# Performance work log

Measured on AMD Instinct MI355X. Metric: run time of the kernel, lower is better.

Reference implementation:

```python
import jax, jax.numpy as jnp
import numpy as np

B, S, E, H = 2, 2048, 768, 12
HD = E // H
EPS = 1e-5


def setup_inputs() -> dict:
    key = jax.random.key(0)
    ks = jax.random.split(key, 7)
    sc_in = 1.0 / np.sqrt(E)
    return {
        "x": jax.random.normal(ks[0], (B, S, E), dtype=jnp.float32),
        "gamma": jnp.ones((E,), dtype=jnp.float32),
        "beta": jnp.zeros((E,), dtype=jnp.float32),
        "Wqkv": jax.random.normal(ks[1], (3 * E, E), dtype=jnp.float32) * sc_in,
        "bqkv": jax.random.normal(ks[2], (3 * E,), dtype=jnp.float32) * 0.01,
        "Wo": jax.random.normal(ks[3], (E, E), dtype=jnp.float32) * sc_in,
        "bo": jax.random.normal(ks[4], (E,), dtype=jnp.float32) * 0.01,
    }


def reference(x, gamma, beta, Wqkv, bqkv, Wo, bo):
    # LayerNorm
    mu = jnp.mean(x, axis=-1, keepdims=True)
    var = jnp.mean(jnp.square(x - mu), axis=-1, keepdims=True)
    xn = (x - mu) * jax.lax.rsqrt(var + EPS) * gamma + beta
    # fused QKV projection; original reshapes to [B,S,H,3*hd] then chunks,
    # i.e. per-head blocks of 3*hd split into q/k/v slices of hd each.
    qkv = (xn @ Wqkv.T + bqkv).reshape(B, S, H, 3, HD)
    q, k, v = qkv[..., 0, :], qkv[..., 1, :], qkv[..., 2, :]  # [B,S,H,hd]
    scores = jnp.einsum("bshd,bthd->bhst", q, k) / np.sqrt(HD)
    attn = jax.nn.softmax(scores, axis=-1)  # [B,H,S,S]
    out = jnp.einsum("bhst,bthd->bshd", attn, v).reshape(B, S, E)
    return out @ Wo.T + bo
```

## Files before the change

kernel.cpp:

```cpp
#include <hip/hip_runtime.h>
#include <math.h>

#define B_  2
#define S_  2048
#define E_  768
#define H_  12
#define HD_ 64
#define M_  (B_ * S_)
#define N3E (3 * E_)

typedef __attribute__((ext_vector_type(8)))  short short8;
typedef __attribute__((ext_vector_type(8)))  _Float16 half8;
typedef __attribute__((ext_vector_type(4)))  _Float16 half4;
typedef __attribute__((ext_vector_type(2)))  _Float16 half2_t;
typedef __attribute__((ext_vector_type(4)))  float floatx4;
typedef __attribute__((ext_vector_type(16))) float floatx16;

#define QSCALE 0.18033688011112042f

__device__ inline unsigned short f2bf(float f) {
  union { float f; unsigned u; } a; a.f = f;
  unsigned r = a.u + 0x7fff + ((a.u >> 16) & 1);
  return (unsigned short)(r >> 16);
}
__device__ inline unsigned short f2bf_fast(float f) {
  union { float f; unsigned u; } a; a.f = f;
  return (unsigned short)((a.u + 0x8000u) >> 16);
}
__device__ inline half2_t pkrtz(float a, float b) {
  return __builtin_bit_cast(half2_t, __builtin_amdgcn_cvt_pkrtz(a, b));
}

__global__ __launch_bounds__(256) void cvt2_kernel(
    const float* __restrict__ w1, const float* __restrict__ w2,
    unsigned short* __restrict__ d1, unsigned short* __restrict__ d2,
    int n1_4, int ntot4) {
  int i = blockIdx.x * 256 + threadIdx.x;
  if (i >= ntot4) return;
  const float* src; unsigned short* dst; int k;
  if (i < n1_4) { src = w1; dst = d1; k = i; }
  else          { src = w2; dst = d2; k = i - n1_4; }
  float4 f = *(const float4*)&src[k * 4];
  ushort4 r;
  r.x = f2bf(f.x); r.y = f2bf(f.y); r.z = f2bf(f.z); r.w = f2bf(f.w);
  *(ushort4*)&dst[k * 4] = r;
}

__global__ __launch_bounds__(256) void ln_kernel(
    const float* __restrict__ x, const float* __restrict__ gamma,
    const float* __restrict__ beta, unsigned short* __restrict__ xnb) {
  const int wv = threadIdx.x >> 6, lane = threadIdx.x & 63;
  const int row = blockIdx.x * 4 + wv;
  const float* xr = x + (size_t)row * E_;

  float4 a = ((const float4*)xr)[lane];
  float4 b = ((const float4*)xr)[lane + 64];
  float4 c = ((const float4*)xr)[lane + 128];

  float s  = (a.x + a.y) + (a.z + a.w) + (b.x + b.y) + (b.z + b.w)
           + (c.x + c.y) + (c.z + c.w);
  float s2 = a.x*a.x + a.y*a.y + a.z*a.z + a.w*a.w
           + b.x*b.x + b.y*b.y + b.z*b.z + b.w*b.w
           + c.x*c.x + c.y*c.y + c.z*c.z + c.w*c.w;
#pragma unroll
  for (int o = 32; o > 0; o >>= 1) {
    s  += __shfl_xor(s, o);
    s2 += __shfl_xor(s2, o);
  }
  const float mu  = s * (1.0f / E_);
  const float var = s2 * (1.0f / E_) - mu * mu;
  const float rs  = rsqrtf(var + 1e-5f);

  const float4* gp = (const float4*)gamma;
  const float4* bp = (const float4*)beta;
  ushort4* xo = (ushort4*)(xnb + (size_t)row * E_);

  float4 vin[3] = {a, b, c};
#pragma unroll
  for (int j = 0; j < 3; j++) {
    float4 g = gp[lane + 64 * j];
    float4 be = bp[lane + 64 * j];
    float4 v = vin[j];
    ushort4 r;
    r.x = f2bf((v.x - mu) * rs * g.x + be.x);
    r.y = f2bf((v.y - mu) * rs * g.y + be.y);
    r.z = f2bf((v.z - mu) * rs * g.z + be.z);
    r.w = f2bf((v.w - mu) * rs * g.w + be.w);
    xo[lane + 64 * j] = r;
  }
}

__global__ __launch_bounds__(256) void bgemm_kernel(
    const unsigned short* __restrict__ A, const unsigned short* __restrict__ Wb,
    const float* __restrict__ bias, int mode,
    unsigned short* __restrict__ qbf, unsigned short* __restrict__ kbf,
    _Float16* __restrict__ vth, float* __restrict__ out) {
  __shared__ __align__(16) unsigned short As[128 * 64];
  __shared__ __align__(16) unsigned short Bs[128 * 64];

  const int t  = threadIdx.x;
  const int ln = t & 63, wv = t >> 6;
  const int lr = ln & 15, lg = ln >> 4;
  const int wr = wv >> 1, wc = wv & 1;
  const int m0 = blockIdx.x * 128, n0 = blockIdx.y * 128;

  const int srow = ln >> 3;
  const int scol = (ln & 7) * 8;

  const unsigned short* Ag = A  + (size_t)(m0 + wv * 32 + srow) * 768 + scol;
  const unsigned short* Bg = Wb + (size_t)(n0 + wv * 32 + srow) * 768 + scol;

  floatx4 acc[4][4];
#pragma unroll
  for (int i = 0; i < 4; i++)
#pragma unroll
    for (int j = 0; j < 4; j++) acc[i][j] = (floatx4){0.f, 0.f, 0.f, 0.f};

  for (int k0 = 0; k0 < 768; k0 += 64) {
    __syncthreads();
#pragma unroll
    for (int j = 0; j < 4; j++) {
      __builtin_amdgcn_global_load_lds(
          (const __attribute__((address_space(1))) void*)(Ag + k0 + j * 8 * 768),
          (__attribute__((address_space(3))) void*)(&As[(wv * 32 + j * 8) * 64]),
          16, 0, 0);
      __builtin_amdgcn_global_load_lds(
          (const __attribute__((address_space(1))) void*)(Bg + k0 + j * 8 * 768),
          (__attribute__((address_space(3))) void*)(&Bs[(wv * 32 + j * 8) * 64]),
          16, 0, 0);
    }
    __syncthreads();

#pragma unroll
    for (int kk = 0; kk < 2; kk++) {
      short8 af[4], bf[4];
#pragma unroll
      for (int i = 0; i < 4; i++)
        af[i] = *(const short8*)&As[(wr * 64 + i * 16 + lr) * 64 + kk * 32 + lg * 8];
#pragma unroll
      for (int j = 0; j < 4; j++)
        bf[j] = *(const short8*)&Bs[(wc * 64 + j * 16 + lr) * 64 + kk * 32 + lg * 8];
#pragma unroll
      for (int i = 0; i < 4; i++)
#pragma unroll
        for (int j = 0; j < 4; j++)
          acc[i][j] = __builtin_amdgcn_mfma_f32_16x16x32_bf16(af[i], bf[j], acc[i][j], 0, 0, 0);
    }
  }

  if (mode == 1) {
#pragma unroll
    for (int i = 0; i < 4; i++) {
      const int grow0 = m0 + wr * 64 + i * 16 + lg * 4;
#pragma unroll
      for (int j = 0; j < 4; j++) {
        const int gcol = n0 + wc * 64 + j * 16 + lr;
        const float bb = bias[gcol];
#pragma unroll
        for (int r = 0; r < 4; r++)
          out[(size_t)(grow0 + r) * E_ + gcol] = acc[i][j][r] + bb;
      }
    }
  } else {
#pragma unroll
    for (int i = 0; i < 4; i++) {
      const int grow0 = m0 + wr * 64 + i * 16 + lg * 4;
      const int bq = grow0 >> 11, s0 = grow0 & 2047;
      const int tb = s0 >> 6, kh = (s0 >> 5) & 1;
#pragma unroll
      for (int j = 0; j < 4; j++) {
        const int n = n0 + wc * 64 + j * 16 + lr;
        const int h = n / 192, w = (n >> 6) % 3, d = n & 63;
        const int bh = bq * H_ + h;
        const float bb = bias[n];
        if (w == 2) {
          const int db = d >> 5, l31v = d & 31;
          const int kc2 = (s0 >> 4) & 1, l5v = (s0 >> 3) & 1, e0 = s0 & 7;
          half2_t h01 = pkrtz(acc[i][j][0] + bb, acc[i][j][1] + bb);
          half2_t h23 = pkrtz(acc[i][j][2] + bb, acc[i][j][3] + bb);
          half4 hv = __builtin_shufflevector(h01, h23, 0, 1, 2, 3);
          const size_t idx =
              ((((((size_t)bh * 32 + tb) * 2 + kh) * 2 + db) * 2 + kc2) * 2 + l5v) * 256
              + (size_t)l31v * 8 + e0;
          *(half4*)&vth[idx] = hv;
        } else {
          unsigned short* dst = (w == 0) ? qbf : kbf;
          const float sc = (w == 0) ? QSCALE : 1.0f;
          const int kc = d >> 4, l5 = (d >> 3) & 1, e = d & 7;
          const size_t basei =
              ((((size_t)bh * 32 + tb) * 2 + kh) * 4 + kc) * 512 + (size_t)l5 * 256 + e;
          const int r0 = (s0 & 31) * 8;
#pragma unroll
          for (int r = 0; r < 4; r++)
            dst[basei + r0 + r * 8] = f2bf_fast((acc[i][j][r] + bb) * sc);
        }
      }
    }
  }
}

#define PROW 40

__global__ __launch_bounds__(256, 4) void attn_kernel(
    const unsigned short* __restrict__ qb, const unsigned short* __restrict__ kb,
    const _Float16* __restrict__ vth, unsigned short* __restrict__ ao) {
  __shared__ __align__(16) unsigned char smem[26112];
  _Float16* Ps = (_Float16*)smem;
  float* C1 = (float*)smem;
  float* C2 = C1 + 3 * 64 * 17;

  const int t = threadIdx.x;
  const int lane = t & 63, wv = t >> 6;
  const int l31 = lane & 31, l5 = lane >> 5;

  const int id = blockIdx.x;
  const int bh = (id & 7) * 3 + ((id >> 3) >> 6);
  const int qt = (id >> 3) & 63;
  const int b = bh / H_, h = bh % H_;
  const int q0 = qt * 32;

  short8 qf[4];
  {
    const unsigned short* qp =
        qb + ((size_t)(bh * 32 + (qt >> 1)) * 2 + (qt & 1)) * 2048 + (size_t)lane * 8;
#pragma unroll
    for (int kc = 0; kc < 4; kc++) qf[kc] = *(const short8*)(qp + kc * 512);
  }

  floatx16 oacc0 = (floatx16)0.0f;
  floatx16 oacc1 = (floatx16)0.0f;
  float lsum = 0.f;

  const unsigned short* kpb =
      kb + (size_t)(bh * 32 + (wv >> 1)) * 4096 + (size_t)(wv & 1) * 2048 + (size_t)lane * 8;
  const _Float16* vpb =
      vth + (size_t)(bh * 32 + (wv >> 1)) * 4096 + (size_t)(wv & 1) * 2048 + (size_t)lane * 8;
  _Float16* PsW = Ps + wv * 32 * PROW;

  short8 kf[4];
  half8 vf[4];
#pragma unroll
  for (int kc = 0; kc < 4; kc++) kf[kc] = *(const short8*)(kpb + kc * 512);
  floatx16 sacc = (floatx16)0.0f;
#pragma unroll
  for (int kc = 0; kc < 4; kc++)
    sacc = __builtin_amdgcn_mfma_f32_32x32x16_bf16(kf[kc], qf[kc], sacc, 0, 0, 0);
#pragma unroll
  for (int kc = 0; kc < 4; kc++) kf[kc] = *(const short8*)(kpb + 8192 + kc * 512);
#pragma unroll
  for (int j = 0; j < 4; j++) vf[j] = *(const half8*)(vpb + j * 512);

  for (int tb = 0; tb < 16; tb++) {
#pragma unroll
    for (int r = 0; r < 16; r++) sacc[r] = exp2f(sacc[r]);
    {
      float s01 = (sacc[0] + sacc[1]) + (sacc[2] + sacc[3]);
      float s23 = (sacc[4] + sacc[5]) + (sacc[6] + sacc[7]);
      float s45 = (sacc[8] + sacc[9]) + (sacc[10] + sacc[11]);
      float s67 = (sacc[12] + sacc[13]) + (sacc[14] + sacc[15]);
      lsum += (s01 + s23) + (s45 + s67);
    }
#pragma unroll
    for (int rq = 0; rq < 4; rq++) {
      half2_t a = pkrtz(sacc[rq * 4 + 0], sacc[rq * 4 + 1]);
      half2_t c = pkrtz(sacc[rq * 4 + 2], sacc[rq * 4 + 3]);
      half4 w = __builtin_shufflevector(a, c, 0, 1, 2, 3);
      *(half4*)&PsW[l31 * PROW + rq * 8 + l5 * 4] = w;
    }
    const _Float16* prd = &PsW[l31 * PROW + l5 * 8];
    half8 pf0 = *(const half8*)(prd);
    half8 pf1 = *(const half8*)(prd + 16);

    oacc0 = __builtin_amdgcn_mfma_f32_32x32x16_f16(vf[0], pf0, oacc0, 0, 0, 0);
    oacc0 = __builtin_amdgcn_mfma_f32_32x32x16_f16(vf[1], pf1, oacc0, 0, 0, 0);
    oacc1 = __builtin_amdgcn_mfma_f32_32x32x16_f16(vf[2], pf0, oacc1, 0, 0, 0);
    oacc1 = __builtin_amdgcn_mfma_f32_32x32x16_f16(vf[3], pf1, oacc1, 0, 0, 0);

    if (tb != 15) {
      const _Float16* vt2 = vpb + (size_t)(tb + 1) * 8192;
#pragma unroll
      for (int j = 0; j < 4; j++) vf[j] = *(const half8*)(vt2 + j * 512);
      sacc = (floatx16)0.0f;
#pragma unroll
      for (int kc = 0; kc < 4; kc++)
        sacc = __builtin_amdgcn_mfma_f32_32x32x16_bf16(kf[kc], qf[kc], sacc, 0, 0, 0);
      const unsigned short* kt2 = kpb + (size_t)((tb + 2) & 15) * 8192;
#pragma unroll
      for (int kc = 0; kc < 4; kc++) kf[kc] = *(const short8*)(kt2 + kc * 512);
    }
  }

  const float l2 = lsum + __shfl_xor(lsum, 32);

  __syncthreads();
  if (wv > 0) {
    float* c = &C1[(size_t)((wv - 1) * 64 + lane) * 17];
#pragma unroll
    for (int j = 0; j < 16; j++) c[j] = oacc0[j];
    c[16] = l2;
  }
  if (wv != 1) {
    const int slot = (wv == 0) ? 0 : wv - 1;
    float* c = &C2[(size_t)(slot * 64 + lane) * 17];
#pragma unroll
    for (int j = 0; j < 16; j++) c[j] = oacc1[j];
    c[16] = l2;
  }
  __syncthreads();
  if (wv < 2) {
    float o[16];
    float L;
    if (wv == 0) {
      L = l2;
#pragma unroll
      for (int j = 0; j < 16; j++) o[j] = oacc0[j];
#pragma unroll
      for (int i = 0; i < 3; i++) {
        const float* c = &C1[(size_t)(i * 64 + lane) * 17];
#pragma unroll
        for (int j = 0; j < 16; j++) o[j] += c[j];
        L += c[16];
      }
    } else {
      L = l2;
#pragma unroll
      for (int j = 0; j < 16; j++) o[j] = oacc1[j];
#pragma unroll
      for (int i = 0; i < 3; i++) {
        const float* c = &C2[(size_t)(i * 64 + lane) * 17];
#pragma unroll
        for (int j = 0; j < 16; j++) o[j] += c[j];
        L += c[16];
      }
    }
    const float inv = 1.0f / L;
    const int row = q0 + l31;
    const int dbase = wv * 32;
    unsigned short* arow = &ao[((size_t)(b * S_ + row)) * E_ + h * HD_ + dbase];
#pragma unroll
    for (int a = 0; a < 4; a++) {
      ushort4 s;
      s.x = f2bf(o[a * 4 + 0] * inv);
      s.y = f2bf(o[a * 4 + 1] * inv);
      s.z = f2bf(o[a * 4 + 2] * inv);
      s.w = f2bf(o[a * 4 + 3] * inv);
      *(ushort4*)&arow[8 * a + 4 * l5] = s;
    }
  }
}

extern "C" void kernel_launch(void* const* d_in, const int* in_sizes, int n_in,
                              void* d_out, int out_size, void* d_ws, size_t ws_size,
                              hipStream_t stream) {
  const float* x     = (const float*)d_in[0];
  const float* gamma = (const float*)d_in[1];
  const float* beta  = (const float*)d_in[2];
  const float* Wqkv  = (const float*)d_in[3];
  const float* bqkv  = (const float*)d_in[4];
  const float* Wo    = (const float*)d_in[5];
  const float* bo    = (const float*)d_in[6];
  float* out = (float*)d_out;

  const size_t SZ = (size_t)M_ * E_;
  unsigned short* xnb = (unsigned short*)d_ws;
  unsigned short* qbf = xnb + SZ;
  unsigned short* kbf = qbf + SZ;
  _Float16*       vth = (_Float16*)(kbf + SZ);
  unsigned short* aob = (unsigned short*)(vth + SZ);
  unsigned short* wqb = aob + SZ;
  unsigned short* wob = wqb + (size_t)N3E * E_;

  const int nq4 = (N3E * E_) / 4;
  const int no4 = (E_ * E_) / 4;
  const int ntot4 = nq4 + no4;
  cvt2_kernel<<<(ntot4 + 255) / 256, 256, 0, stream>>>(Wqkv, Wo, wqb, wob, nq4, ntot4);

  ln_kernel<<<M_ / 4, 256, 0, stream>>>(x, gamma, beta, xnb);

  dim3 g_qkv(M_ / 128, N3E / 128);
  bgemm_kernel<<<g_qkv, 256, 0, stream>>>(xnb, wqb, bqkv, 0, qbf, kbf, vth, nullptr);

  attn_kernel<<<1536, 256, 0, stream>>>(qbf, kbf, vth, aob);

  dim3 g_out(M_ / 128, E_ / 128);
  bgemm_kernel<<<g_out, 256, 0, stream>>>(aob, wob, bo, 1, nullptr, nullptr, nullptr, out);
}
```

Before: 182.7 us.

## Narrow GEMM N-tile to 64 and vectorize Q/K epilogue via transposed MFMA

The GEMM block tile shrinks from 128x128 to 128x64, so each block covers exactly one Q, K or V head slice and the head/type decode becomes uniform per block. For Q and K tiles the MFMA operands are swapped, which yields a transposed accumulator, and results are written as ushort4 vectors into a new per-tile layout instead of scalar scattered stores. The attention kernel's Q and K loads are changed to read this layout with paired short4 loads. The smaller tile doubles the block count, which helps occupancy, but it lowers reuse of the A operand, and the output GEMM also uses the narrower tile.

```diff
diff --git a/kernel.cpp b/kernel.cpp
--- a/kernel.cpp
+++ b/kernel.cpp
@@ -10,6 +10,7 @@
 #define N3E (3 * E_)
 
 typedef __attribute__((ext_vector_type(8)))  short short8;
+typedef __attribute__((ext_vector_type(4)))  short short4v;
 typedef __attribute__((ext_vector_type(8)))  _Float16 half8;
 typedef __attribute__((ext_vector_type(4)))  _Float16 half4;
 typedef __attribute__((ext_vector_type(2)))  _Float16 half2_t;
@@ -96,104 +97,120 @@
     unsigned short* __restrict__ qbf, unsigned short* __restrict__ kbf,
     _Float16* __restrict__ vth, float* __restrict__ out) {
   __shared__ __align__(16) unsigned short As[128 * 64];
-  __shared__ __align__(16) unsigned short Bs[128 * 64];
+  __shared__ __align__(16) unsigned short Bs[64 * 64];
 
   const int t  = threadIdx.x;
   const int ln = t & 63, wv = t >> 6;
   const int lr = ln & 15, lg = ln >> 4;
-  const int wr = wv >> 1, wc = wv & 1;
-  const int m0 = blockIdx.x * 128, n0 = blockIdx.y * 128;
+  const int m0 = blockIdx.x * 128, n0 = blockIdx.y * 64;
+  const int w  = (mode == 1) ? 3 : ((n0 >> 6) % 3);
 
   const int srow = ln >> 3;
   const int scol = (ln & 7) * 8;
 
   const unsigned short* Ag = A  + (size_t)(m0 + wv * 32 + srow) * 768 + scol;
-  const unsigned short* Bg = Wb + (size_t)(n0 + wv * 32 + srow) * 768 + scol;
-
-  floatx4 acc[4][4];
-#pragma unroll
-  for (int i = 0; i < 4; i++)
+  const unsigned short* Bg = Wb + (size_t)(n0 + wv * 16 + srow) * 768 + scol;
+
+  floatx4 acc[2][4];
+#pragma unroll
+  for (int i = 0; i < 2; i++)
 #pragma unroll
     for (int j = 0; j < 4; j++) acc[i][j] = (floatx4){0.f, 0.f, 0.f, 0.f};
 
   for (int k0 = 0; k0 < 768; k0 += 64) {
     __syncthreads();
 #pragma unroll
-    for (int j = 0; j < 4; j++) {
+    for (int j = 0; j < 4; j++)
       __builtin_amdgcn_global_load_lds(
           (const __attribute__((address_space(1))) void*)(Ag + k0 + j * 8 * 768),
           (__attribute__((address_space(3))) void*)(&As[(wv * 32 + j * 8) * 64]),
           16, 0, 0);
+#pragma unroll
+    for (int j = 0; j < 2; j++)
       __builtin_amdgcn_global_load_lds(
           (const __attribute__((address_space(1))) void*)(Bg + k0 + j * 8 * 768),
-          (__attribute__((address_space(3))) void*)(&Bs[(wv * 32 + j * 8) * 64]),
+          (__attribute__((address_space(3))) void*)(&Bs[(wv * 16 + j * 8) * 64]),
           16, 0, 0);
-    }
     __syncthreads();
 
 #pragma unroll
     for (int kk = 0; kk < 2; kk++) {
-      short8 af[4], bf[4];
-#pragma unroll
-      for (int i = 0; i < 4; i++)
-        af[i] = *(const short8*)&As[(wr * 64 + i * 16 + lr) * 64 + kk * 32 + lg * 8];
+      short8 af[2], bf[4];
+#pragma unroll
+      for (int i = 0; i < 2; i++)
+        af[i] = *(const short8*)&As[(wv * 32 + i * 16 + lr) * 64 + kk * 32 + lg * 8];
 #pragma unroll
       for (int j = 0; j < 4; j++)
-        bf[j] = *(const short8*)&Bs[(wc * 64 + j * 16 + lr) * 64 + kk * 32 + lg * 8];
-#pragma unroll
-      for (int i = 0; i < 4; i++)
-#pragma unroll
-        for (int j = 0; j < 4; j++)
-          acc[i][j] = __builtin_amdgcn_mfma_f32_16x16x32_bf16(af[i], bf[j], acc[i][j], 0, 0, 0);
+        bf[j] = *(const short8*)&Bs[(j * 16 + lr) * 64 + kk * 32 + lg * 8];
+      if (w < 2) {
+#pragma unroll
+        for (int i = 0; i < 2; i++)
+#pragma unroll
+          for (int j = 0; j < 4; j++)
+            acc[i][j] = __builtin_amdgcn_mfma_f32_16x16x32_bf16(bf[j], af[i], acc[i][j], 0, 0, 0);
+      } else {
+#pragma unroll
+        for (int i = 0; i < 2; i++)
+#pragma unroll
+          for (int j = 0; j < 4; j++)
+            acc[i][j] = __builtin_amdgcn_mfma_f32_16x16x32_bf16(af[i], bf[j], acc[i][j], 0, 0, 0);
+      }
     }
   }
 
   if (mode == 1) {
 #pragma unroll
-    for (int i = 0; i < 4; i++) {
-      const int grow0 = m0 + wr * 64 + i * 16 + lg * 4;
+    for (int i = 0; i < 2; i++) {
+      const int grow0 = m0 + wv * 32 + i * 16 + lg * 4;
 #pragma unroll
       for (int j = 0; j < 4; j++) {
-        const int gcol = n0 + wc * 64 + j * 16 + lr;
+        const int gcol = n0 + j * 16 + lr;
         const float bb = bias[gcol];
 #pragma unroll
         for (int r = 0; r < 4; r++)
           out[(size_t)(grow0 + r) * E_ + gcol] = acc[i][j][r] + bb;
       }
     }
+  } else if (w < 2) {
+    const int h = n0 / 192;
+    const int bh = (m0 >> 11) * H_ + h;
+    unsigned short* dst = (w == 0) ? qbf : kbf;
+    const float sc = (w == 0) ? QSCALE : 1.0f;
+#pragma unroll
+    for (int i = 0; i < 2; i++) {
+      const int s = (m0 & 2047) + wv * 32 + i * 16 + lr;
+      const size_t rowb = (size_t)bh * 131072 + (size_t)(s >> 5) * 2048 + (s & 31) * 4;
+#pragma unroll
+      for (int j = 0; j < 4; j++) {
+        float4 b4 = *(const float4*)&bias[n0 + j * 16 + lg * 4];
+        ushort4 r;
+        r.x = f2bf_fast((acc[i][j][0] + b4.x) * sc);
+        r.y = f2bf_fast((acc[i][j][1] + b4.y) * sc);
+        r.z = f2bf_fast((acc[i][j][2] + b4.z) * sc);
+        r.w = f2bf_fast((acc[i][j][3] + b4.w) * sc);
+        *(ushort4*)&dst[rowb + (size_t)(j * 4 + lg) * 128] = r;
+      }
+    }
   } else {
-#pragma unroll
-    for (int i = 0; i < 4; i++) {
-      const int grow0 = m0 + wr * 64 + i * 16 + lg * 4;
-      const int bq = grow0 >> 11, s0 = grow0 & 2047;
+    const int h = n0 / 192;
+    const int bh = (m0 >> 11) * H_ + h;
+#pragma unroll
+    for (int i = 0; i < 2; i++) {
+      const int s0 = (m0 & 2047) + wv * 32 + i * 16 + lg * 4;
       const int tb = s0 >> 6, kh = (s0 >> 5) & 1;
+      const int kc2 = (s0 >> 4) & 1, l5v = (s0 >> 3) & 1, e0 = s0 & 7;
 #pragma unroll
       for (int j = 0; j < 4; j++) {
-        const int n = n0 + wc * 64 + j * 16 + lr;
-        const int h = n / 192, w = (n >> 6) % 3, d = n & 63;
-        const int bh = bq * H_ + h;
-        const float bb = bias[n];
-        if (w == 2) {
-          const int db = d >> 5, l31v = d & 31;
-          const int kc2 = (s0 >> 4) & 1, l5v = (s0 >> 3) & 1, e0 = s0 & 7;
-          half2_t h01 = pkrtz(acc[i][j][0] + bb, acc[i][j][1] + bb);
-          half2_t h23 = pkrtz(acc[i][j][2] + bb, acc[i][j][3] + bb);
-          half4 hv = __builtin_shufflevector(h01, h23, 0, 1, 2, 3);
-          const size_t idx =
-              ((((((size_t)bh * 32 + tb) * 2 + kh) * 2 + db) * 2 + kc2) * 2 + l5v) * 256
-              + (size_t)l31v * 8 + e0;
-          *(half4*)&vth[idx] = hv;
-        } else {
-          unsigned short* dst = (w == 0) ? qbf : kbf;
-          const float sc = (w == 0) ? QSCALE : 1.0f;
-          const int kc = d >> 4, l5 = (d >> 3) & 1, e = d & 7;
-          const size_t basei =
-              ((((size_t)bh * 32 + tb) * 2 + kh) * 4 + kc) * 512 + (size_t)l5 * 256 + e;
-          const int r0 = (s0 & 31) * 8;
-#pragma unroll
-          for (int r = 0; r < 4; r++)
-            dst[basei + r0 + r * 8] = f2bf_fast((acc[i][j][r] + bb) * sc);
-        }
+        const int d = j * 16 + lr;
+        const int db = d >> 5, l31v = d & 31;
+        const float bb = bias[n0 + d];
+        half2_t h01 = pkrtz(acc[i][j][0] + bb, acc[i][j][1] + bb);
+        half2_t h23 = pkrtz(acc[i][j][2] + bb, acc[i][j][3] + bb);
+        half4 hv = __builtin_shufflevector(h01, h23, 0, 1, 2, 3);
+        const size_t idx =
+            ((((((size_t)bh * 32 + tb) * 2 + kh) * 2 + db) * 2 + kc2) * 2 + l5v) * 256
+            + (size_t)l31v * 8 + e0;
+        *(half4*)&vth[idx] = hv;
       }
     }
   }
@@ -221,10 +238,13 @@
 
   short8 qf[4];
   {
-    const unsigned short* qp =
-        qb + ((size_t)(bh * 32 + (qt >> 1)) * 2 + (qt & 1)) * 2048 + (size_t)lane * 8;
-#pragma unroll
-    for (int kc = 0; kc < 4; kc++) qf[kc] = *(const short8*)(qp + kc * 512);
+    const unsigned short* qp = qb + (size_t)bh * 131072 + (size_t)qt * 2048 + l31 * 4;
+#pragma unroll
+    for (int kc = 0; kc < 4; kc++) {
+      short4v a = *(const short4v*)(qp + (kc * 4 + l5 * 2) * 128);
+      short4v b2 = *(const short4v*)(qp + (kc * 4 + l5 * 2) * 128 + 128);
+      qf[kc] = __builtin_shufflevector(a, b2, 0, 1, 2, 3, 4, 5, 6, 7);
+    }
   }
 
   floatx16 oacc0 = (floatx16)0.0f;
@@ -232,21 +252,30 @@
   float lsum = 0.f;
 
   const unsigned short* kpb =
-      kb + (size_t)(bh * 32 + (wv >> 1)) * 4096 + (size_t)(wv & 1) * 2048 + (size_t)lane * 8;
+      kb + (size_t)bh * 131072 + (size_t)(2 * (wv >> 1) + (wv & 1)) * 2048 + l31 * 4;
   const _Float16* vpb =
       vth + (size_t)(bh * 32 + (wv >> 1)) * 4096 + (size_t)(wv & 1) * 2048 + (size_t)lane * 8;
   _Float16* PsW = Ps + wv * 32 * PROW;
 
+#define LDK(kfv, tb2)                                                          \
+  {                                                                            \
+    const unsigned short* _p = kpb + (size_t)(tb2) * 8192;                     \
+    _Pragma("unroll")                                                          \
+    for (int kc = 0; kc < 4; kc++) {                                           \
+      short4v _a = *(const short4v*)(_p + (kc * 4 + l5 * 2) * 128);            \
+      short4v _b = *(const short4v*)(_p + (kc * 4 + l5 * 2) * 128 + 128);      \
+      kfv[kc] = __builtin_shufflevector(_a, _b, 0, 1, 2, 3, 4, 5, 6, 7);       \
+    }                                                                          \
+  }
+
   short8 kf[4];
   half8 vf[4];
-#pragma unroll
-  for (int kc = 0; kc < 4; kc++) kf[kc] = *(const short8*)(kpb + kc * 512);
+  LDK(kf, 0);
   floatx16 sacc = (floatx16)0.0f;
 #pragma unroll
   for (int kc = 0; kc < 4; kc++)
     sacc = __builtin_amdgcn_mfma_f32_32x32x16_bf16(kf[kc], qf[kc], sacc, 0, 0, 0);
-#pragma unroll
-  for (int kc = 0; kc < 4; kc++) kf[kc] = *(const short8*)(kpb + 8192 + kc * 512);
+  LDK(kf, 1);
 #pragma unroll
   for (int j = 0; j < 4; j++) vf[j] = *(const half8*)(vpb + j * 512);
 
@@ -284,9 +313,7 @@
 #pragma unroll
       for (int kc = 0; kc < 4; kc++)
         sacc = __builtin_amdgcn_mfma_f32_32x32x16_bf16(kf[kc], qf[kc], sacc, 0, 0, 0);
-      const unsigned short* kt2 = kpb + (size_t)((tb + 2) & 15) * 8192;
-#pragma unroll
-      for (int kc = 0; kc < 4; kc++) kf[kc] = *(const short8*)(kt2 + kc * 512);
+      LDK(kf, (tb + 2) & 15);
     }
   }
 
@@ -377,11 +404,11 @@
 
   ln_kernel<<<M_ / 4, 256, 0, stream>>>(x, gamma, beta, xnb);
 
-  dim3 g_qkv(M_ / 128, N3E / 128);
+  dim3 g_qkv(M_ / 128, N3E / 64);
   bgemm_kernel<<<g_qkv, 256, 0, stream>>>(xnb, wqb, bqkv, 0, qbf, kbf, vth, nullptr);
 
   attn_kernel<<<1536, 256, 0, stream>>>(qbf, kbf, vth, aob);
 
-  dim3 g_out(M_ / 128, E_ / 128);
+  dim3 g_out(M_ / 128, E_ / 64);
   bgemm_kernel<<<g_out, 256, 0, stream>>>(aob, wob, bo, 1, nullptr, nullptr, nullptr, out);
 }
```

Result: faster. 175.1 us (-4.2%).
